# Kernel optimization log

Measured on AMD Instinct MI355X. Metric: run time of the kernel, lower is better.

Reference implementation:

```python
import jax, jax.numpy as jnp
import numpy as np

N_NODES = 100000
D_IN = 64
HID = 128
N_EDGES = 1600000
N_LBL = 500000


def setup_inputs() -> dict:
    key = jax.random.key(0)
    ks = jax.random.split(key, 16)
    s = 0.05
    return {
        "x": jax.random.normal(ks[0], (N_NODES, D_IN), dtype=jnp.float32),
        "edge_index": jax.random.randint(ks[1], (2, N_EDGES), 0, N_NODES, dtype=jnp.int64),
        "edge_label_index": jax.random.randint(ks[2], (2, N_LBL), 0, N_NODES, dtype=jnp.int64),
        # SAGEConv1: lin_l (aggregated neighbors, with bias), lin_r (root, no bias)
        "w1l": jax.random.normal(ks[3], (D_IN, HID), dtype=jnp.float32) * s,
        "b1l": jnp.zeros((HID,), dtype=jnp.float32),
        "w1r": jax.random.normal(ks[4], (D_IN, HID), dtype=jnp.float32) * s,
        # SAGEConv2
        "w2l": jax.random.normal(ks[5], (HID, HID), dtype=jnp.float32) * s,
        "b2l": jnp.zeros((HID,), dtype=jnp.float32),
        "w2r": jax.random.normal(ks[6], (HID, HID), dtype=jnp.float32) * s,
        # EdgeDecoder
        "dw1": jax.random.normal(ks[7], (2 * HID, HID), dtype=jnp.float32) * s,
        "db1": jnp.zeros((HID,), dtype=jnp.float32),
        "dw2": jax.random.normal(ks[8], (HID, 1), dtype=jnp.float32) * s,
        "db2": jnp.zeros((1,), dtype=jnp.float32),
    }


def _sage_conv(x, src, dst, inv_deg, wl, bl, wr):
    # mean-aggregate neighbor features at destination nodes, then linear
    agg = jax.ops.segment_sum(x[src], dst, num_segments=N_NODES)  # [N, d]
    mean = agg * inv_deg[:, None]
    return mean @ wl + bl + x @ wr


def reference(x, edge_index, edge_label_index,
              w1l, b1l, w1r, w2l, b2l, w2r, dw1, db1, dw2, db2):
    src, dst = edge_index[0], edge_index[1]
    deg = jax.ops.segment_sum(jnp.ones((N_EDGES,), jnp.float32), dst,
                              num_segments=N_NODES)
    inv_deg = jnp.where(deg > 0, 1.0 / jnp.maximum(deg, 1.0), 0.0)

    # encoder: SAGEConv -> relu -> SAGEConv
    h = jax.nn.relu(_sage_conv(x, src, dst, inv_deg, w1l, b1l, w1r))
    z = _sage_conv(h, src, dst, inv_deg, w2l, b2l, w2r)  # [N, HID]

    # decoder: gather endpoint embeddings per label edge, concat, MLP
    zz = jnp.concatenate([z[edge_label_index[0]], z[edge_label_index[1]]],
                         axis=-1)  # [E_lbl, 2*HID]
    h2 = jax.nn.relu(zz @ dw1 + db1)
    out = h2 @ dw2 + db2  # [E_lbl, 1]
    return out.reshape(-1)
```

## Files before the change

### kernel.cpp

```cpp
#include <hip/hip_runtime.h>

#define N_NODES 100000
#define D_IN 64
#define HID 128
#define N_EDGES 1600000
#define N_LBL 500000
#define NBUCK 196
#define NSCANB 98
#define LCAP 3072

typedef __attribute__((ext_vector_type(8))) short bf16x8;
typedef __attribute__((ext_vector_type(4))) float f32x4;

__device__ inline unsigned short f2bf(float f) {
  unsigned int u = __float_as_uint(f);
  return (unsigned short)((u + 0x7FFFu + ((u >> 16) & 1u)) >> 16);
}
__device__ inline float bf_lo(unsigned int w) { return __uint_as_float(w << 16); }
__device__ inline float bf_hi(unsigned int w) { return __uint_as_float(w & 0xFFFF0000u); }
__device__ inline float bfs(short s) {
  return __uint_as_float(((unsigned int)(unsigned short)s) << 16);
}

__global__ __launch_bounds__(256) void k_deg(const int* __restrict__ dst,
                                             int* __restrict__ deg) {
  int e = blockIdx.x * 256 + threadIdx.x;
  if (e < N_EDGES) atomicAdd(&deg[dst[e]], 1);
}

__global__ __launch_bounds__(1024) void k_scan_a(const int* __restrict__ deg,
                                                 int* __restrict__ rowptr,
                                                 float* __restrict__ inv,
                                                 int* __restrict__ bsum) {
  __shared__ int s_wsum[16];
  const int lane = threadIdx.x & 63;
  const int wid = threadIdx.x >> 6;
  const int i = blockIdx.x * 1024 + threadIdx.x;
  int v = (i < N_NODES) ? deg[i] : 0;
  int x = v;
#pragma unroll
  for (int off = 1; off < 64; off <<= 1) {
    int t = __shfl_up(x, off);
    if (lane >= off) x += t;
  }
  if (lane == 63) s_wsum[wid] = x;
  __syncthreads();
  if (wid == 0 && lane < 16) {
    int ws = s_wsum[lane];
    int y = ws;
#pragma unroll
    for (int off = 1; off < 16; off <<= 1) {
      int t = __shfl_up(y, off);
      if (lane >= off) y += t;
    }
    s_wsum[lane] = y - ws;
    if (lane == 15) bsum[blockIdx.x] = y;
  }
  __syncthreads();
  if (i < N_NODES) {
    rowptr[i] = s_wsum[wid] + x - v;
    inv[i] = v > 0 ? 1.0f / (float)v : 0.0f;
  }
}

__global__ __launch_bounds__(128) void k_scan_b(int* __restrict__ bsum,
                                                int* __restrict__ rowptr) {
  __shared__ int s_w;
  const int tid = threadIdx.x;
  const int lane = tid & 63, wid = tid >> 6;
  int v = (tid < NSCANB) ? bsum[tid] : 0;
  int x = v;
#pragma unroll
  for (int off = 1; off < 64; off <<= 1) {
    int t = __shfl_up(x, off);
    if (lane >= off) x += t;
  }
  if (wid == 0 && lane == 63) s_w = x;
  __syncthreads();
  int incl = x + (wid == 1 ? s_w : 0);
  if (tid < NSCANB) bsum[tid] = incl - v;
  if (tid == NSCANB - 1) rowptr[N_NODES] = incl;
}

__global__ __launch_bounds__(1024) void k_scan_c(int* __restrict__ rowptr,
                                                 const int* __restrict__ bsum,
                                                 int* __restrict__ gcursor) {
  const int i = blockIdx.x * 1024 + threadIdx.x;
  if (i < N_NODES) {
    int r = rowptr[i] + bsum[blockIdx.x];
    rowptr[i] = r;
    if ((i & 511) == 0) gcursor[i >> 9] = r;
  }
}

__global__ __launch_bounds__(256) void k_bin(const int* __restrict__ src,
                                             const int* __restrict__ dst,
                                             int* __restrict__ gcursor,
                                             int* __restrict__ binned) {
  __shared__ int hist[NBUCK];
  __shared__ int base[NBUCK];
  const int tid = threadIdx.x;
  const int e0 = blockIdx.x * 4096 + tid;
  for (int t = tid; t < NBUCK; t += 256) hist[t] = 0;
  __syncthreads();

  int w[16], bk[16], rk[16];
#pragma unroll
  for (int i = 0; i < 16; ++i) {
    int e = e0 + i * 256;
    if (e < N_EDGES) {
      int s = src[e], d = dst[e];
      bk[i] = d >> 9;
      w[i] = (s << 9) | (d & 511);
      rk[i] = atomicAdd(&hist[bk[i]], 1);
    } else {
      bk[i] = -1;
    }
  }
  __syncthreads();
  for (int t = tid; t < NBUCK; t += 256)
    base[t] = hist[t] > 0 ? atomicAdd(&gcursor[t], hist[t]) : 0;
  __syncthreads();
#pragma unroll
  for (int i = 0; i < 16; ++i)
    if (bk[i] >= 0) binned[base[bk[i]] + rk[i]] = w[i];
}

__global__ __launch_bounds__(256) void k_fill2(const int* __restrict__ rowptr,
                                               const int* __restrict__ binned,
                                               int* __restrict__ csr) {
  __shared__ int lcur[512];
  const int b = blockIdx.x;
  const int nb = b << 9;
  const int nn = min(512, N_NODES - nb);
  for (int i = threadIdx.x; i < nn; i += 256) lcur[i] = rowptr[nb + i];
  __syncthreads();
  const int beg = rowptr[nb], end = rowptr[nb + nn];
  for (int e = beg + threadIdx.x; e < end; e += 256) {
    int w = binned[e];
    int pos = atomicAdd(&lcur[w & 511], 1);
    csr[pos] = w >> 9;
  }
}

__global__ __launch_bounds__(256) void k_lbl_bin(const int* __restrict__ ls,
                                                 const int* __restrict__ ld,
                                                 int* __restrict__ lblcnt,
                                                 int2* __restrict__ lbin) {
  __shared__ int hist[NBUCK];
  __shared__ int base[NBUCK];
  const int tid = threadIdx.x;
  const int e0 = blockIdx.x * 4096 + tid;
  for (int t = tid; t < NBUCK; t += 256) hist[t] = 0;
  __syncthreads();

  int dd[16], pk[16], bk[16], rk[16];
#pragma unroll
  for (int i = 0; i < 16; ++i) {
    int e = e0 + i * 256;
    if (e < N_LBL) {
      int s = ls[e];
      dd[i] = ld[e];
      bk[i] = s >> 9;
      pk[i] = (e << 9) | (s & 511);
      rk[i] = atomicAdd(&hist[bk[i]], 1);
    } else {
      bk[i] = -1;
    }
  }
  __syncthreads();
  for (int t = tid; t < NBUCK; t += 256)
    base[t] = hist[t] > 0 ? atomicAdd(&lblcnt[t], hist[t]) : 0;
  __syncthreads();
#pragma unroll
  for (int i = 0; i < 16; ++i)
    if (bk[i] >= 0) {
      int2 rec = {dd[i], pk[i]};
      lbin[(long)bk[i] * LCAP + base[bk[i]] + rk[i]] = rec;
    }
}

__global__ __launch_bounds__(256) void k_prep(
    const float* __restrict__ x, const float* __restrict__ w1l,
    const float* __restrict__ w1r, const float* __restrict__ w2l,
    const float* __restrict__ w2r, const float* __restrict__ dw1,
    unsigned short* __restrict__ x16, unsigned short* __restrict__ w1lt,
    unsigned short* __restrict__ w1rt, unsigned short* __restrict__ w2lt,
    unsigned short* __restrict__ w2rt, unsigned short* __restrict__ dw1t) {
  long gid = (long)blockIdx.x * 256 + threadIdx.x;
  if (gid < 1600000) {
    long i = gid * 4;
    float4 v = *(const float4*)&x[i];
    ushort4 q = {f2bf(v.x), f2bf(v.y), f2bf(v.z), f2bf(v.w)};
    *(ushort4*)&x16[i] = q;
    return;
  }
  long idx = gid - 1600000;
  if (idx < 8192) { int n = idx >> 6, k = idx & 63; w1lt[idx] = f2bf(w1l[k * 128 + n]); return; }
  idx -= 8192;
  if (idx < 8192) { int n = idx >> 6, k = idx & 63; w1rt[idx] = f2bf(w1r[k * 128 + n]); return; }
  idx -= 8192;
  if (idx < 16384) { int n = idx >> 7, k = idx & 127; w2lt[idx] = f2bf(w2l[k * 128 + n]); return; }
  idx -= 16384;
  if (idx < 16384) { int n = idx >> 7, k = idx & 127; w2rt[idx] = f2bf(w2r[k * 128 + n]); return; }
  idx -= 16384;
  if (idx < 32768) {
    int n = idx >> 7, k = idx & 127;
    dw1t[idx] = f2bf(n < 128 ? dw1[k * 128 + n] : dw1[(k + 128) * 128 + (n - 128)]);
  }
}

__global__ __launch_bounds__(256) void k_agg64(const int* __restrict__ rowptr,
                                               const int* __restrict__ csr,
                                               const unsigned short* __restrict__ f16,
                                               const float* __restrict__ inv,
                                               unsigned short* __restrict__ out16) {
  const int lane = threadIdx.x & 63;
  const int n = blockIdx.x * 4 + (threadIdx.x >> 6);
  const int beg = rowptr[n], end = rowptr[n + 1];
  float acc = 0.0f;
  int j = beg;
  for (; j + 4 <= end; j += 4) {
    int s0 = csr[j], s1 = csr[j + 1], s2 = csr[j + 2], s3 = csr[j + 3];
    float f0 = bf_lo((unsigned int)f16[(long)s0 * 64 + lane]);
    float f1 = bf_lo((unsigned int)f16[(long)s1 * 64 + lane]);
    float f2 = bf_lo((unsigned int)f16[(long)s2 * 64 + lane]);
    float f3 = bf_lo((unsigned int)f16[(long)s3 * 64 + lane]);
    acc += f0; acc += f1; acc += f2; acc += f3;
  }
  for (; j < end; ++j) acc += bf_lo((unsigned int)f16[(long)csr[j] * 64 + lane]);
  out16[(long)n * 64 + lane] = f2bf(acc * inv[n]);
}

__global__ __launch_bounds__(256) void k_agg128(const int* __restrict__ rowptr,
                                                const int* __restrict__ csr,
                                                const unsigned short* __restrict__ f16,
                                                const float* __restrict__ inv,
                                                unsigned short* __restrict__ out16) {
  const int lane = threadIdx.x & 63;
  const int wv = threadIdx.x >> 6;
  const int g = lane >> 4;
  const int q = lane & 15;
  const int n = (blockIdx.x * 4 + wv) * 4 + g;
  const int beg = rowptr[n], end = rowptr[n + 1];
  float acc[8] = {0, 0, 0, 0, 0, 0, 0, 0};
  int j = beg;
  for (; j + 2 <= end; j += 2) {
    int s0 = csr[j], s1 = csr[j + 1];
    bf16x8 v0 = *(const bf16x8*)(f16 + (long)s0 * 128 + q * 8);
    bf16x8 v1 = *(const bf16x8*)(f16 + (long)s1 * 128 + q * 8);
#pragma unroll
    for (int i = 0; i < 8; ++i) acc[i] += bfs(v0[i]);
#pragma unroll
    for (int i = 0; i < 8; ++i) acc[i] += bfs(v1[i]);
  }
  if (j < end) {
    bf16x8 v0 = *(const bf16x8*)(f16 + (long)csr[j] * 128 + q * 8);
#pragma unroll
    for (int i = 0; i < 8; ++i) acc[i] += bfs(v0[i]);
  }
  float iv = inv[n];
  bf16x8 r;
#pragma unroll
  for (int i = 0; i < 8; ++i) r[i] = (short)f2bf(acc[i] * iv);
  *(bf16x8*)(out16 + (long)n * 128 + q * 8) = r;
}

__global__ __launch_bounds__(256) void k_l1(
    const unsigned short* __restrict__ m1, const unsigned short* __restrict__ x16,
    const unsigned short* __restrict__ w1lt, const unsigned short* __restrict__ w1rt,
    const float* __restrict__ b1l, unsigned short* __restrict__ h16) {
  const int l = threadIdx.x & 63;
  const int w = threadIdx.x >> 6;
  const int cl = l & 15;
  const int kh = l >> 4;
  const int wrow0 = blockIdx.x * 128 + w * 32;
  int ar0 = wrow0 + cl;      if (ar0 >= N_NODES) ar0 = N_NODES - 1;
  int ar1 = wrow0 + 16 + cl; if (ar1 >= N_NODES) ar1 = N_NODES - 1;

  f32x4 acc[2][8];
#pragma unroll
  for (int t = 0; t < 2; ++t)
#pragma unroll
    for (int nt = 0; nt < 8; ++nt) acc[t][nt] = (f32x4){0.f, 0.f, 0.f, 0.f};

#pragma unroll
  for (int s = 0; s < 2; ++s) {
    const int ko = s * 32 + kh * 8;
    bf16x8 am0 = *(const bf16x8*)(m1 + (long)ar0 * 64 + ko);
    bf16x8 ax0 = *(const bf16x8*)(x16 + (long)ar0 * 64 + ko);
    bf16x8 am1 = *(const bf16x8*)(m1 + (long)ar1 * 64 + ko);
    bf16x8 ax1 = *(const bf16x8*)(x16 + (long)ar1 * 64 + ko);
#pragma unroll
    for (int nt = 0; nt < 8; ++nt) {
      bf16x8 bl = *(const bf16x8*)(w1lt + (long)(nt * 16 + cl) * 64 + ko);
      bf16x8 br = *(const bf16x8*)(w1rt + (long)(nt * 16 + cl) * 64 + ko);
      acc[0][nt] = __builtin_amdgcn_mfma_f32_16x16x32_bf16(am0, bl, acc[0][nt], 0, 0, 0);
      acc[0][nt] = __builtin_amdgcn_mfma_f32_16x16x32_bf16(ax0, br, acc[0][nt], 0, 0, 0);
      acc[1][nt] = __builtin_amdgcn_mfma_f32_16x16x32_bf16(am1, bl, acc[1][nt], 0, 0, 0);
      acc[1][nt] = __builtin_amdgcn_mfma_f32_16x16x32_bf16(ax1, br, acc[1][nt], 0, 0, 0);
    }
  }

#pragma unroll
  for (int t = 0; t < 2; ++t)
#pragma unroll
    for (int nt = 0; nt < 8; ++nt) {
      float b = b1l[nt * 16 + cl];
#pragma unroll
      for (int i = 0; i < 4; ++i) {
        int r = wrow0 + t * 16 + kh * 4 + i;
        if (r < N_NODES)
          h16[(long)r * 128 + nt * 16 + cl] = f2bf(fmaxf(acc[t][nt][i] + b, 0.0f));
      }
    }
}

__global__ __launch_bounds__(128) void k_l2uv(
    const unsigned short* __restrict__ m2, const unsigned short* __restrict__ h16,
    const unsigned short* __restrict__ w2lt, const unsigned short* __restrict__ w2rt,
    const float* __restrict__ b2l, const unsigned short* __restrict__ dw1t,
    const float* __restrict__ db1,
    unsigned short* __restrict__ u16, unsigned short* __restrict__ v16) {
  __shared__ unsigned short s_z[2][32 * 128];
  const int l = threadIdx.x & 63;
  const int w = threadIdx.x >> 6;
  char* zb = (char*)s_z[w];
  const int cl = l & 15;
  const int kh = l >> 4;
  const int wrow0 = blockIdx.x * 64 + w * 32;
  int ar0 = wrow0 + cl;      if (ar0 >= N_NODES) ar0 = N_NODES - 1;
  int ar1 = wrow0 + 16 + cl; if (ar1 >= N_NODES) ar1 = N_NODES - 1;

  f32x4 acc[2][8];
#pragma unroll
  for (int t = 0; t < 2; ++t)
#pragma unroll
    for (int nt = 0; nt < 8; ++nt) acc[t][nt] = (f32x4){0.f, 0.f, 0.f, 0.f};

#pragma unroll
  for (int s = 0; s < 4; ++s) {
    const int ko = s * 32 + kh * 8;
    bf16x8 am0 = *(const bf16x8*)(m2 + (long)ar0 * 128 + ko);
    bf16x8 ah0 = *(const bf16x8*)(h16 + (long)ar0 * 128 + ko);
    bf16x8 am1 = *(const bf16x8*)(m2 + (long)ar1 * 128 + ko);
    bf16x8 ah1 = *(const bf16x8*)(h16 + (long)ar1 * 128 + ko);
#pragma unroll
    for (int nt = 0; nt < 8; ++nt) {
      bf16x8 bl = *(const bf16x8*)(w2lt + (long)(nt * 16 + cl) * 128 + ko);
      bf16x8 br = *(const bf16x8*)(w2rt + (long)(nt * 16 + cl) * 128 + ko);
      acc[0][nt] = __builtin_amdgcn_mfma_f32_16x16x32_bf16(am0, bl, acc[0][nt], 0, 0, 0);
      acc[0][nt] = __builtin_amdgcn_mfma_f32_16x16x32_bf16(ah0, br, acc[0][nt], 0, 0, 0);
      acc[1][nt] = __builtin_amdgcn_mfma_f32_16x16x32_bf16(am1, bl, acc[1][nt], 0, 0, 0);
      acc[1][nt] = __builtin_amdgcn_mfma_f32_16x16x32_bf16(ah1, br, acc[1][nt], 0, 0, 0);
    }
  }

#pragma unroll
  for (int t = 0; t < 2; ++t)
#pragma unroll
    for (int nt = 0; nt < 8; ++nt) {
      float b = b2l[nt * 16 + cl];
#pragma unroll
      for (int i = 0; i < 4; ++i) {
        int zr = t * 16 + kh * 4 + i;
        int byte = (zr * 256 + (nt * 16 + cl) * 2) ^ ((zr & 7) << 4);
        *(unsigned short*)(zb + byte) = f2bf(acc[t][nt][i] + b);
      }
    }

  f32x4 uu[2][8];
#pragma unroll
  for (int t = 0; t < 2; ++t)
#pragma unroll
    for (int nt = 0; nt < 8; ++nt) uu[t][nt] = (f32x4){0.f, 0.f, 0.f, 0.f};
#pragma unroll
  for (int s = 0; s < 4; ++s) {
    const int zr0 = cl;
    const int zr1 = 16 + cl;
    bf16x8 az0 = *(const bf16x8*)(zb + ((zr0 * 256 + s * 64 + kh * 16) ^ ((zr0 & 7) << 4)));
    bf16x8 az1 = *(const bf16x8*)(zb + ((zr1 * 256 + s * 64 + kh * 16) ^ ((zr1 & 7) << 4)));
#pragma unroll
    for (int nt = 0; nt < 8; ++nt) {
      bf16x8 bu = *(const bf16x8*)(dw1t + (long)(nt * 16 + cl) * 128 + s * 32 + kh * 8);
      uu[0][nt] = __builtin_amdgcn_mfma_f32_16x16x32_bf16(az0, bu, uu[0][nt], 0, 0, 0);
      uu[1][nt] = __builtin_amdgcn_mfma_f32_16x16x32_bf16(az1, bu, uu[1][nt], 0, 0, 0);
    }
  }
#pragma unroll
  for (int t = 0; t < 2; ++t)
#pragma unroll
    for (int nt = 0; nt < 8; ++nt) {
      float bb = db1[nt * 16 + cl];
#pragma unroll
      for (int i = 0; i < 4; ++i) {
        int r = wrow0 + t * 16 + kh * 4 + i;
        if (r < N_NODES) u16[(long)r * 128 + nt * 16 + cl] = f2bf(uu[t][nt][i] + bb);
      }
    }

#pragma unroll
  for (int t = 0; t < 2; ++t)
#pragma unroll
    for (int nt = 0; nt < 8; ++nt) uu[t][nt] = (f32x4){0.f, 0.f, 0.f, 0.f};
#pragma unroll
  for (int s = 0; s < 4; ++s) {
    const int zr0 = cl;
    const int zr1 = 16 + cl;
    bf16x8 az0 = *(const bf16x8*)(zb + ((zr0 * 256 + s * 64 + kh * 16) ^ ((zr0 & 7) << 4)));
    bf16x8 az1 = *(const bf16x8*)(zb + ((zr1 * 256 + s * 64 + kh * 16) ^ ((zr1 & 7) << 4)));
#pragma unroll
    for (int nt = 0; nt < 8; ++nt) {
      bf16x8 bv = *(const bf16x8*)(dw1t + (long)((nt + 8) * 16 + cl) * 128 + s * 32 + kh * 8);
      uu[0][nt] = __builtin_amdgcn_mfma_f32_16x16x32_bf16(az0, bv, uu[0][nt], 0, 0, 0);
      uu[1][nt] = __builtin_amdgcn_mfma_f32_16x16x32_bf16(az1, bv, uu[1][nt], 0, 0, 0);
    }
  }
#pragma unroll
  for (int t = 0; t < 2; ++t)
#pragma unroll
    for (int nt = 0; nt < 8; ++nt)
#pragma unroll
      for (int i = 0; i < 4; ++i) {
        int r = wrow0 + t * 16 + kh * 4 + i;
        if (r < N_NODES) v16[(long)r * 128 + nt * 16 + cl] = f2bf(uu[t][nt][i]);
      }
}

__global__ __launch_bounds__(256) void k_edge2(
    const int* __restrict__ lblcnt, const int2* __restrict__ lbin,
    const unsigned short* __restrict__ u16, const unsigned short* __restrict__ v16,
    const float* __restrict__ dw2, const float* __restrict__ db2,
    float* __restrict__ out) {
  const int lane = threadIdx.x & 63;
  const int wv = threadIdx.x >> 6;
  const int g = lane >> 4;
  const int q = lane & 15;
  const int b = blockIdx.x / (LCAP / 16);
  const int chunk = blockIdx.x % (LCAP / 16);
  const int idx = chunk * 16 + wv * 4 + g;
  if (idx >= lblcnt[b]) return;
  int2 rec = lbin[(long)b * LCAP + idx];
  int d = rec.x;
  int s = (b << 9) + (rec.y & 511);
  int e = rec.y >> 9;

  bf16x8 uu = *(const bf16x8*)(u16 + (long)s * 128 + q * 8);
  bf16x8 vv = *(const bf16x8*)(v16 + (long)d * 128 + q * 8);
  float4 w0 = *(const float4*)&dw2[q * 8];
  float4 w1 = *(const float4*)&dw2[q * 8 + 4];
  float w8[8] = {w0.x, w0.y, w0.z, w0.w, w1.x, w1.y, w1.z, w1.w};
  float sum = 0.0f;
#pragma unroll
  for (int i = 0; i < 8; ++i) {
    float h = fmaxf(bfs(uu[i]) + bfs(vv[i]), 0.0f);
    sum = fmaf(h, w8[i], sum);
  }
  sum += __shfl_xor(sum, 1);
  sum += __shfl_xor(sum, 2);
  sum += __shfl_xor(sum, 4);
  sum += __shfl_xor(sum, 8);
  if (q == 0) out[e] = sum + db2[0];
}

extern "C" void kernel_launch(void* const* d_in, const int* in_sizes, int n_in,
                              void* d_out, int out_size, void* d_ws, size_t ws_size,
                              hipStream_t stream) {
  const float* x   = (const float*)d_in[0];
  const int*   ei  = (const int*)d_in[1];
  const int*   eli = (const int*)d_in[2];
  const float* w1l = (const float*)d_in[3];
  const float* b1l = (const float*)d_in[4];
  const float* w1r = (const float*)d_in[5];
  const float* w2l = (const float*)d_in[6];
  const float* b2l = (const float*)d_in[7];
  const float* w2r = (const float*)d_in[8];
  const float* dw1 = (const float*)d_in[9];
  const float* db1 = (const float*)d_in[10];
  const float* dw2 = (const float*)d_in[11];
  const float* db2 = (const float*)d_in[12];
  float* out = (float*)d_out;

  char* wsb = (char*)d_ws;
  float* inv     = (float*)(wsb + 0);
  int*   deg_i   = (int*)(wsb + 400000);
  int*   rowptr  = (int*)(wsb + 800000);
  int*   gcursor = (int*)(wsb + 1200032);
  int*   csr     = (int*)(wsb + 1201056);
  int*   binned  = (int*)(wsb + 7601056);
  unsigned short* x16  = (unsigned short*)(wsb + 14001056);
  unsigned short* m1   = (unsigned short*)(wsb + 26801056);
  unsigned short* u16  = (unsigned short*)(wsb + 14001056);
  unsigned short* h16  = (unsigned short*)(wsb + 39601056);
  unsigned short* m2   = (unsigned short*)(wsb + 65201056);
  unsigned short* v16  = (unsigned short*)(wsb + 90801056);
  unsigned short* w1lt = (unsigned short*)(wsb + 116401056);
  unsigned short* w1rt = (unsigned short*)(wsb + 116417440);
  unsigned short* w2lt = (unsigned short*)(wsb + 116433824);
  unsigned short* w2rt = (unsigned short*)(wsb + 116466592);
  unsigned short* dw1t = (unsigned short*)(wsb + 116499360);
  int*   bsum    = (int*)(wsb + 116564896);
  int*   lblcnt  = (int*)(wsb + 116565408);
  int2*  lbin    = (int2*)(wsb + 116566208);

  const int* srcp = ei;
  const int* dstp = ei + N_EDGES;
  const int* lsp  = eli;
  const int* ldp  = eli + N_LBL;

  hipMemsetAsync(deg_i, 0, N_NODES * sizeof(int), stream);
  hipMemsetAsync(lblcnt, 0, NBUCK * sizeof(int), stream);
  k_deg<<<N_EDGES / 256, 256, 0, stream>>>(dstp, deg_i);
  k_scan_a<<<NSCANB, 1024, 0, stream>>>(deg_i, rowptr, inv, bsum);
  k_scan_b<<<1, 128, 0, stream>>>(bsum, rowptr);
  k_scan_c<<<NSCANB, 1024, 0, stream>>>(rowptr, bsum, gcursor);
  k_bin<<<(N_EDGES + 4095) / 4096, 256, 0, stream>>>(srcp, dstp, gcursor, binned);
  k_fill2<<<NBUCK, 256, 0, stream>>>(rowptr, binned, csr);
  k_lbl_bin<<<(N_LBL + 4095) / 4096, 256, 0, stream>>>(lsp, ldp, lblcnt, lbin);
  k_prep<<<(1681920 + 255) / 256, 256, 0, stream>>>(
      x, w1l, w1r, w2l, w2r, dw1, x16, w1lt, w1rt, w2lt, w2rt, dw1t);

  k_agg64<<<N_NODES / 4, 256, 0, stream>>>(rowptr, csr, x16, inv, m1);
  k_l1<<<(N_NODES + 127) / 128, 256, 0, stream>>>(m1, x16, w1lt, w1rt, b1l, h16);

  k_agg128<<<N_NODES / 16, 256, 0, stream>>>(rowptr, csr, h16, inv, m2);
  k_l2uv<<<(N_NODES + 63) / 64, 128, 0, stream>>>(m2, h16, w2lt, w2rt, b2l, dw1t, db1, u16, v16);

  k_edge2<<<NBUCK * (LCAP / 16), 256, 0, stream>>>(lblcnt, lbin, u16, v16, dw2, db2, out);
}
```

Baseline: 444.5 us.

## Split l2uv work across two waves per 32-row tile with shared z

k_l2uv now gives each block a 32-row tile, and its two waves split the output columns of the layer-2 GEMM. They share the z tile through LDS behind a __syncthreads, and one wave then computes u while the other computes v. Before, each wave handled its own 32 rows and computed both u and v serially. The change halves per-wave accumulator registers and doubles the grid, which should raise occupancy and parallelism. The cost is each wave reloading the A operands and a block barrier, and bounds checks are dropped because N_NODES divides evenly by 32.

```diff
diff --git a/kernel.cpp b/kernel.cpp
--- a/kernel.cpp
+++ b/kernel.cpp
@@ -322,21 +322,21 @@
     const float* __restrict__ b2l, const unsigned short* __restrict__ dw1t,
     const float* __restrict__ db1,
     unsigned short* __restrict__ u16, unsigned short* __restrict__ v16) {
-  __shared__ unsigned short s_z[2][32 * 128];
+  __shared__ unsigned short s_z[32 * 128];
+  char* zb = (char*)s_z;
   const int l = threadIdx.x & 63;
   const int w = threadIdx.x >> 6;
-  char* zb = (char*)s_z[w];
   const int cl = l & 15;
   const int kh = l >> 4;
-  const int wrow0 = blockIdx.x * 64 + w * 32;
-  int ar0 = wrow0 + cl;      if (ar0 >= N_NODES) ar0 = N_NODES - 1;
-  int ar1 = wrow0 + 16 + cl; if (ar1 >= N_NODES) ar1 = N_NODES - 1;
-
-  f32x4 acc[2][8];
+  const int row0 = blockIdx.x * 32;
+  const int ar0 = row0 + cl;
+  const int ar1 = row0 + 16 + cl;
+
+  f32x4 acc[2][4];
 #pragma unroll
   for (int t = 0; t < 2; ++t)
 #pragma unroll
-    for (int nt = 0; nt < 8; ++nt) acc[t][nt] = (f32x4){0.f, 0.f, 0.f, 0.f};
+    for (int nt = 0; nt < 4; ++nt) acc[t][nt] = (f32x4){0.f, 0.f, 0.f, 0.f};
 
 #pragma unroll
   for (int s = 0; s < 4; ++s) {
@@ -346,29 +346,33 @@
     bf16x8 am1 = *(const bf16x8*)(m2 + (long)ar1 * 128 + ko);
     bf16x8 ah1 = *(const bf16x8*)(h16 + (long)ar1 * 128 + ko);
 #pragma unroll
-    for (int nt = 0; nt < 8; ++nt) {
+    for (int nt4 = 0; nt4 < 4; ++nt4) {
+      const int nt = w * 4 + nt4;
       bf16x8 bl = *(const bf16x8*)(w2lt + (long)(nt * 16 + cl) * 128 + ko);
       bf16x8 br = *(const bf16x8*)(w2rt + (long)(nt * 16 + cl) * 128 + ko);
-      acc[0][nt] = __builtin_amdgcn_mfma_f32_16x16x32_bf16(am0, bl, acc[0][nt], 0, 0, 0);
-      acc[0][nt] = __builtin_amdgcn_mfma_f32_16x16x32_bf16(ah0, br, acc[0][nt], 0, 0, 0);
-      acc[1][nt] = __builtin_amdgcn_mfma_f32_16x16x32_bf16(am1, bl, acc[1][nt], 0, 0, 0);
-      acc[1][nt] = __builtin_amdgcn_mfma_f32_16x16x32_bf16(ah1, br, acc[1][nt], 0, 0, 0);
+      acc[0][nt4] = __builtin_amdgcn_mfma_f32_16x16x32_bf16(am0, bl, acc[0][nt4], 0, 0, 0);
+      acc[0][nt4] = __builtin_amdgcn_mfma_f32_16x16x32_bf16(ah0, br, acc[0][nt4], 0, 0, 0);
+      acc[1][nt4] = __builtin_amdgcn_mfma_f32_16x16x32_bf16(am1, bl, acc[1][nt4], 0, 0, 0);
+      acc[1][nt4] = __builtin_amdgcn_mfma_f32_16x16x32_bf16(ah1, br, acc[1][nt4], 0, 0, 0);
     }
   }
 
 #pragma unroll
   for (int t = 0; t < 2; ++t)
 #pragma unroll
-    for (int nt = 0; nt < 8; ++nt) {
+    for (int nt4 = 0; nt4 < 4; ++nt4) {
+      const int nt = w * 4 + nt4;
       float b = b2l[nt * 16 + cl];
 #pragma unroll
       for (int i = 0; i < 4; ++i) {
         int zr = t * 16 + kh * 4 + i;
         int byte = (zr * 256 + (nt * 16 + cl) * 2) ^ ((zr & 7) << 4);
-        *(unsigned short*)(zb + byte) = f2bf(acc[t][nt][i] + b);
+        *(unsigned short*)(zb + byte) = f2bf(acc[t][nt4][i] + b);
       }
     }
-
+  __syncthreads();
+
+  const int bofs = w * 128;
   f32x4 uu[2][8];
 #pragma unroll
   for (int t = 0; t < 2; ++t)
@@ -382,49 +386,24 @@
     bf16x8 az1 = *(const bf16x8*)(zb + ((zr1 * 256 + s * 64 + kh * 16) ^ ((zr1 & 7) << 4)));
 #pragma unroll
     for (int nt = 0; nt < 8; ++nt) {
-      bf16x8 bu = *(const bf16x8*)(dw1t + (long)(nt * 16 + cl) * 128 + s * 32 + kh * 8);
-      uu[0][nt] = __builtin_amdgcn_mfma_f32_16x16x32_bf16(az0, bu, uu[0][nt], 0, 0, 0);
-      uu[1][nt] = __builtin_amdgcn_mfma_f32_16x16x32_bf16(az1, bu, uu[1][nt], 0, 0, 0);
-    }
-  }
+      bf16x8 bw = *(const bf16x8*)(dw1t + (long)(bofs + nt * 16 + cl) * 128 + s * 32 + kh * 8);
+      uu[0][nt] = __builtin_amdgcn_mfma_f32_16x16x32_bf16(az0, bw, uu[0][nt], 0, 0, 0);
+      uu[1][nt] = __builtin_amdgcn_mfma_f32_16x16x32_bf16(az1, bw, uu[1][nt], 0, 0, 0);
+    }
+  }
+
+  unsigned short* outp = w ? v16 : u16;
 #pragma unroll
   for (int t = 0; t < 2; ++t)
 #pragma unroll
     for (int nt = 0; nt < 8; ++nt) {
-      float bb = db1[nt * 16 + cl];
+      float bb = w ? 0.0f : db1[nt * 16 + cl];
 #pragma unroll
       for (int i = 0; i < 4; ++i) {
-        int r = wrow0 + t * 16 + kh * 4 + i;
-        if (r < N_NODES) u16[(long)r * 128 + nt * 16 + cl] = f2bf(uu[t][nt][i] + bb);
+        int r = row0 + t * 16 + kh * 4 + i;
+        outp[(long)r * 128 + nt * 16 + cl] = f2bf(uu[t][nt][i] + bb);
       }
     }
-
-#pragma unroll
-  for (int t = 0; t < 2; ++t)
-#pragma unroll
-    for (int nt = 0; nt < 8; ++nt) uu[t][nt] = (f32x4){0.f, 0.f, 0.f, 0.f};
-#pragma unroll
-  for (int s = 0; s < 4; ++s) {
-    const int zr0 = cl;
-    const int zr1 = 16 + cl;
-    bf16x8 az0 = *(const bf16x8*)(zb + ((zr0 * 256 + s * 64 + kh * 16) ^ ((zr0 & 7) << 4)));
-    bf16x8 az1 = *(const bf16x8*)(zb + ((zr1 * 256 + s * 64 + kh * 16) ^ ((zr1 & 7) << 4)));
-#pragma unroll
-    for (int nt = 0; nt < 8; ++nt) {
-      bf16x8 bv = *(const bf16x8*)(dw1t + (long)((nt + 8) * 16 + cl) * 128 + s * 32 + kh * 8);
-      uu[0][nt] = __builtin_amdgcn_mfma_f32_16x16x32_bf16(az0, bv, uu[0][nt], 0, 0, 0);
-      uu[1][nt] = __builtin_amdgcn_mfma_f32_16x16x32_bf16(az1, bv, uu[1][nt], 0, 0, 0);
-    }
-  }
-#pragma unroll
-  for (int t = 0; t < 2; ++t)
-#pragma unroll
-    for (int nt = 0; nt < 8; ++nt)
-#pragma unroll
-      for (int i = 0; i < 4; ++i) {
-        int r = wrow0 + t * 16 + kh * 4 + i;
-        if (r < N_NODES) v16[(long)r * 128 + nt * 16 + cl] = f2bf(uu[t][nt][i]);
-      }
 }
 
 __global__ __launch_bounds__(256) void k_edge2(
@@ -524,7 +503,7 @@
   k_l1<<<(N_NODES + 127) / 128, 256, 0, stream>>>(m1, x16, w1lt, w1rt, b1l, h16);
 
   k_agg128<<<N_NODES / 16, 256, 0, stream>>>(rowptr, csr, h16, inv, m2);
-  k_l2uv<<<(N_NODES + 63) / 64, 128, 0, stream>>>(m2, h16, w2lt, w2rt, b2l, dw1t, db1, u16, v16);
+  k_l2uv<<<N_NODES / 32, 128, 0, stream>>>(m2, h16, w2lt, w2rt, b2l, dw1t, db1, u16, v16);
 
   k_edge2<<<NBUCK * (LCAP / 16), 256, 0, stream>>>(lblcnt, lbin, u16, v16, dw2, db2, out);
 }
```

Result: no change. 447.6 us (+0.7%).
